# Kernel optimization log

Measured on AMD Instinct MI355X. Metric: run time of the kernel, lower is better.

The kernel has to match this reference:

```python
import jax, jax.numpy as jnp
import numpy as np

D_IN = 2048
D_OUT = 2048
NUM_HEADS = 32
NUM_KV_GROUPS = 8
HEAD_DIM = D_OUT // NUM_HEADS          # 64
GROUP_SIZE = NUM_HEADS // NUM_KV_GROUPS  # 4
BATCH = 2
SEQ = 2048


def _rope(x, cos, sin):
    # x: [b, h, s, d]; cos/sin: [s, d]
    d = x.shape[-1]
    x1, x2 = x[..., : d // 2], x[..., d // 2:]
    rotated = jnp.concatenate((-x2, x1), axis=-1)
    return x * cos[None, None, :, :] + rotated * sin[None, None, :, :]


def setup_inputs() -> dict:
    key = jax.random.key(0)
    ks = jax.random.split(key, 8)
    x = jax.random.normal(ks[0], (BATCH, SEQ, D_IN), dtype=jnp.float32)
    cos = jax.random.normal(ks[1], (SEQ, HEAD_DIM), dtype=jnp.float32)
    sin = jax.random.normal(ks[2], (SEQ, HEAD_DIM), dtype=jnp.float32)
    # causal mask: True above the diagonal = masked out
    mask = jnp.triu(jnp.ones((SEQ, SEQ), dtype=jnp.bool_), k=1)
    s = 0.02
    Wq = jax.random.normal(ks[3], (D_IN, D_OUT), dtype=jnp.float32) * s
    Wk = jax.random.normal(ks[4], (D_IN, NUM_KV_GROUPS * HEAD_DIM), dtype=jnp.float32) * s
    Wv = jax.random.normal(ks[5], (D_IN, NUM_KV_GROUPS * HEAD_DIM), dtype=jnp.float32) * s
    Wo = jax.random.normal(ks[6], (D_OUT, D_OUT), dtype=jnp.float32) * s
    return {"x": x, "cos": cos, "sin": sin, "mask": mask,
            "Wq": Wq, "Wk": Wk, "Wv": Wv, "Wo": Wo}


def reference(x, cos, sin, mask, Wq, Wk, Wv, Wo):
    b, s, _ = x.shape
    # projections (Linear, no bias): weights stored as [d_in, d_out]
    q = (x @ Wq).reshape(b, s, NUM_HEADS, HEAD_DIM).transpose(0, 2, 1, 3)      # [b,H,s,d]
    k = (x @ Wk).reshape(b, s, NUM_KV_GROUPS, HEAD_DIM).transpose(0, 2, 1, 3)  # [b,G,s,d]
    v = (x @ Wv).reshape(b, s, NUM_KV_GROUPS, HEAD_DIM).transpose(0, 2, 1, 3)  # [b,G,s,d]
    q = _rope(q, cos, sin)
    k = _rope(k, cos, sin)
    # GQA broadcast: repeat each KV group group_size times along head axis
    k = jnp.repeat(k, GROUP_SIZE, axis=1)  # [b,H,s,d]
    v = jnp.repeat(v, GROUP_SIZE, axis=1)  # [b,H,s,d]
    scores = jnp.einsum('bhqd,bhkd->bhqk', q, k)
    scores = jnp.where(mask[None, None, :, :], -jnp.inf, scores)
    # original scales AFTER masking: softmax(scores / sqrt(head_dim)); -inf stays -inf
    attn = jax.nn.softmax(scores * (1.0 / np.sqrt(HEAD_DIM)), axis=-1)
    ctx = jnp.einsum('bhqk,bhkd->bqhd', attn, v).reshape(b, s, D_OUT)
    return ctx @ Wo
```

## Files before the change

kernel.cpp:

```cpp
#include <hip/hip_runtime.h>
#include <hip/hip_fp16.h>

#define SEQ    2048
#define DIN    2048
#define DOUT   2048
#define NH     32
#define NKV    8
#define HD     64
#define BB     2

typedef _Float16 half_t;
typedef __attribute__((ext_vector_type(8))) _Float16 half8;
typedef __attribute__((ext_vector_type(4))) _Float16 half4;
typedef __attribute__((ext_vector_type(2))) __fp16   fp16x2;
typedef __attribute__((ext_vector_type(4))) float    floatx4;

union H8U { half8 h; int u[4]; };
union H2I { fp16x2 h; int i; };

#if __has_builtin(__builtin_amdgcn_exp2f)
#define EXP2F(x) __builtin_amdgcn_exp2f(x)
#else
#define EXP2F(x) __expf((x) * 0.6931471805599453f)
#endif

__device__ __forceinline__ void gload16(void* l, const void* g) {
    __builtin_amdgcn_global_load_lds(
        (const __attribute__((address_space(1))) void*)g,
        (__attribute__((address_space(3))) void*)l, 16, 0, 0);
}

__global__ void cast_f2h(const float* __restrict__ in, half_t* __restrict__ out, int n4) {
    int i = blockIdx.x * blockDim.x + threadIdx.x;
    if (i < n4) {
        float4 v = ((const float4*)in)[i];
        half4 h;
        h[0] = (half_t)v.x; h[1] = (half_t)v.y; h[2] = (half_t)v.z; h[3] = (half_t)v.w;
        ((half4*)out)[i] = h;
    }
}

__global__ __launch_bounds__(256) void tcast(const float* __restrict__ in, half_t* __restrict__ out,
                                             int Kd, int Nd) {
    __shared__ float T[32][33];
    int x0 = blockIdx.x * 32, y0 = blockIdx.y * 32;
    int tx = threadIdx.x & 31, ty = threadIdx.x >> 5;
    #pragma unroll
    for (int j = 0; j < 4; j++)
        T[ty + j * 8][tx] = in[(size_t)(y0 + ty + j * 8) * Nd + x0 + tx];
    __syncthreads();
    #pragma unroll
    for (int j = 0; j < 4; j++)
        out[(size_t)(x0 + ty + j * 8) * Kd + y0 + tx] = (half_t)T[tx][ty + j * 8];
}

__device__ __forceinline__ void gemm128_core(
    const half_t* __restrict__ A, const half_t* __restrict__ Bt,
    int m0, int n0, half_t* As, half_t* Bs, floatx4 (&acc)[4][4])
{
    const int tid = threadIdx.x, wave = tid >> 6, lane = tid & 63;
    const int quad = lane >> 4, l15 = lane & 15;
    const int wm = (wave >> 1) * 64, wn = (wave & 1) * 64;
    const int K = DIN;

    const half_t* pa[4]; const half_t* pb[4]; int ldso[4];
    #pragma unroll
    for (int is = 0; is < 4; is++) {
        int s  = is * 256 + tid;
        int kb = s >> 9, s1 = s & 511;
        int p  = s1 >> 3, sc = s1 & 7;
        int c  = sc ^ (p & 7);
        int row  = 2 * p + (c >> 2);
        int koff = kb * 32 + (c & 3) * 8;
        pa[is] = A  + (size_t)(m0 + row) * K + koff;
        pb[is] = Bt + (size_t)(n0 + row) * K + koff;
        ldso[is] = (is * 256 + wave * 64) * 8;
    }
    int aoff[4], boff[4];
    #pragma unroll
    for (int m = 0; m < 4; m++) {
        int r = wm + m * 16 + l15, p = r >> 1;
        aoff[m] = p * 64 + ((((r & 1) * 4 + quad) ^ (p & 7)) * 8);
        int rn = wn + m * 16 + l15, pn = rn >> 1;
        boff[m] = pn * 64 + ((((rn & 1) * 4 + quad) ^ (pn & 7)) * 8);
    }

    for (int k0 = 0; k0 < K; k0 += 64) {
        __syncthreads();
        #pragma unroll
        for (int is = 0; is < 4; is++) {
            gload16(As + ldso[is], pa[is] + k0);
            gload16(Bs + ldso[is], pb[is] + k0);
        }
        __syncthreads();
        half8 af[4][2], bf[4][2];
        #pragma unroll
        for (int i = 0; i < 4; i++) {
            af[i][0] = *(const half8*)(As + aoff[i]);
            af[i][1] = *(const half8*)(As + 4096 + aoff[i]);
            bf[i][0] = *(const half8*)(Bs + boff[i]);
            bf[i][1] = *(const half8*)(Bs + 4096 + boff[i]);
        }
        #pragma unroll
        for (int i = 0; i < 4; i++)
            #pragma unroll
            for (int j = 0; j < 4; j++)
                #pragma unroll
                for (int ks = 0; ks < 2; ks++)
                    acc[i][j] = __builtin_amdgcn_mfma_f32_16x16x32_f16(af[i][ks], bf[j][ks], acc[i][j], 0, 0, 0);
    }
}

__global__ __launch_bounds__(256) void gemm_qkv(
    const half_t* __restrict__ A, const half_t* __restrict__ Bt,
    const float* __restrict__ cosb, const float* __restrict__ sinb,
    half_t* __restrict__ Qh, half_t* __restrict__ Kh, half_t* __restrict__ Vt)
{
    __shared__ half_t As[8192];
    __shared__ half_t Bs[8192];
    const int bid = blockIdx.x;
    const int wg  = (bid & 7) * 96 + (bid >> 3);
    const int m0  = (wg & 31) * 128;
    const int n0  = (wg >> 5) * 128;

    floatx4 acc[4][4] = {};
    gemm128_core(A, Bt, m0, n0, As, Bs, acc);

    const int tid = threadIdx.x, wave = tid >> 6, lane = tid & 63;
    const int quad = lane >> 4, l15 = lane & 15;
    const int wm = (wave >> 1) * 64, wn = (wave & 1) * 64;
    const int headg = (n0 + wn) >> 6;
    const int b = m0 >> 11;
    const int s_base = (m0 & 2047) + wm + quad * 4;

    if (headg < 32) {
        half_t* outp = Qh + (size_t)(b * NH + headg) * SEQ * 64;
        #pragma unroll
        for (int i = 0; i < 4; i++)
            #pragma unroll
            for (int j = 0; j < 4; j++) {
                int d = j * 16 + l15;
                #pragma unroll
                for (int r = 0; r < 4; r++)
                    outp[(size_t)(s_base + i * 16 + r) * 64 + d] = (half_t)acc[i][j][r];
            }
    } else if (headg < 40) {
        half_t* outp = Kh + (size_t)(b * NKV + (headg - 32)) * SEQ * 64;
        #pragma unroll
        for (int i = 0; i < 4; i++)
            #pragma unroll
            for (int r = 0; r < 4; r++) {
                int s = s_base + i * 16 + r;
                #pragma unroll
                for (int j = 0; j < 2; j++) {
                    int d = j * 16 + l15;
                    float x1 = acc[i][j][r], x2 = acc[i][j + 2][r];
                    float c1 = cosb[s * 64 + d],      s1 = sinb[s * 64 + d];
                    float c2 = cosb[s * 64 + d + 32], s2 = sinb[s * 64 + d + 32];
                    outp[(size_t)s * 64 + d]      = (half_t)(x1 * c1 - x2 * s1);
                    outp[(size_t)s * 64 + d + 32] = (half_t)(x2 * c2 + x1 * s2);
                }
            }
    } else {
        half_t* vtp = Vt + (size_t)(b * NKV + (headg - 40)) * 64 * SEQ;
        #pragma unroll
        for (int i = 0; i < 4; i++) {
            int s = s_base + i * 16;
            #pragma unroll
            for (int j = 0; j < 4; j++) {
                int d = j * 16 + l15;
                half4 hv;
                hv[0] = (half_t)acc[i][j][0];
                hv[1] = (half_t)acc[i][j][1];
                hv[2] = (half_t)acc[i][j][2];
                hv[3] = (half_t)acc[i][j][3];
                *(half4*)(vtp + (size_t)d * SEQ + s) = hv;
            }
        }
    }
}

__global__ __launch_bounds__(256) void gemm_tn_f(
    const half_t* __restrict__ A, const half_t* __restrict__ Bt,
    float* __restrict__ C)
{
    __shared__ half_t As[8192];
    __shared__ half_t Bs[8192];
    const int bid = blockIdx.x;
    const int wg  = (bid & 7) * 64 + (bid >> 3);
    const int m0  = (wg & 31) * 128;
    const int n0  = (wg >> 5) * 128;

    floatx4 acc[4][4] = {};
    gemm128_core(A, Bt, m0, n0, As, Bs, acc);

    const int tid = threadIdx.x, wave = tid >> 6, lane = tid & 63;
    const int quad = lane >> 4, l15 = lane & 15;
    const int wm = (wave >> 1) * 64, wn = (wave & 1) * 64;
    #pragma unroll
    for (int i = 0; i < 4; i++) {
        int row = m0 + wm + i * 16 + quad * 4;
        #pragma unroll
        for (int j = 0; j < 4; j++) {
            int col = n0 + wn + j * 16 + l15;
            #pragma unroll
            for (int r = 0; r < 4; r++)
                C[(size_t)(row + r) * DOUT + col] = acc[i][j][r];
        }
    }
}

__global__ __launch_bounds__(256, 4) void attn(
    const half_t* __restrict__ Qh, const half_t* __restrict__ Kh,
    const half_t* __restrict__ Vt, const float* __restrict__ cosb,
    const float* __restrict__ sinb, half_t* __restrict__ ctx)
{
    __shared__ half_t Ks[2][4096];
    __shared__ half_t Vs[2][4096];

    const int tid = threadIdx.x, wave = tid >> 6, lane = tid & 63;
    const int quad = lane >> 4, l15 = lane & 15;
    const int bid = blockIdx.x;
    const int k  = bid >> 8;
    const int u  = bid & 255;
    const int q2 = u & 3;
    const int bh = u >> 2;
    const int qt = (k == 0) ? 15 - 2 * q2 : (k == 1) ? 2 * q2
                 : (k == 2) ? 14 - 2 * q2 : 2 * q2 + 1;
    const int b  = bh >> 5;
    const int h  = bh & 31;
    const int g  = h >> 2;
    const int q0 = qt * 128;
    const int wm = wave * 32;

    const half_t* kp = Kh + (size_t)(b * NKV + g) * SEQ * 64;
    const half_t* vp = Vt + (size_t)(b * NKV + g) * 64 * SEQ;

    half8 qf[2][2];
    {
        const float sc = 0.125f * 1.44269504088896f;
        const half_t* qpp = Qh + ((size_t)(b * NH + h) * SEQ + q0 + wm) * 64;
        #pragma unroll
        for (int mf = 0; mf < 2; mf++) {
            int s = q0 + wm + mf * 16 + l15;
            const float* cp = cosb + s * 64 + quad * 8;
            const float* sp = sinb + s * 64 + quad * 8;
            half8 xa = *(const half8*)(qpp + (size_t)(mf * 16 + l15) * 64 + quad * 8);
            half8 xb = *(const half8*)(qpp + (size_t)(mf * 16 + l15) * 64 + 32 + quad * 8);
            float4 c1a = *(const float4*)(cp),      c1b = *(const float4*)(cp + 4);
            float4 s1a = *(const float4*)(sp),      s1b = *(const float4*)(sp + 4);
            float4 c2a = *(const float4*)(cp + 32), c2b = *(const float4*)(cp + 36);
            float4 s2a = *(const float4*)(sp + 32), s2b = *(const float4*)(sp + 36);
            #pragma unroll
            for (int t = 0; t < 8; t++) {
                float cc1 = (t < 4) ? ((const float*)&c1a)[t] : ((const float*)&c1b)[t - 4];
                float ss1 = (t < 4) ? ((const float*)&s1a)[t] : ((const float*)&s1b)[t - 4];
                float cc2 = (t < 4) ? ((const float*)&c2a)[t] : ((const float*)&c2b)[t - 4];
                float ss2 = (t < 4) ? ((const float*)&s2a)[t] : ((const float*)&s2b)[t - 4];
                float x1 = (float)xa[t], x2 = (float)xb[t];
                qf[mf][0][t] = (half_t)((x1 * cc1 - x2 * ss1) * sc);
                qf[mf][1][t] = (half_t)((x2 * cc2 + x1 * ss2) * sc);
            }
        }
    }

    int koff[2], voff[2], lo[2];
    #pragma unroll
    for (int is = 0; is < 2; is++) {
        int s = is * 256 + tid;
        int p = s >> 3, c = (s & 7) ^ (p & 7);
        koff[is] = p * 64 + c * 8;
        voff[is] = p * SEQ + c * 8;
        lo[is]   = (is * 256 + wave * 64) * 8;
    }

    float m_i[2], l_i[2];
    m_i[0] = m_i[1] = -__builtin_inff();
    l_i[0] = l_i[1] = 0.f;
    floatx4 o[2][4] = {};

    const int ntiles = 2 * qt + 2;
    #pragma unroll
    for (int is = 0; is < 2; is++) {
        gload16(&Ks[0][lo[is]], kp + koff[is]);
        gload16(&Vs[0][lo[is]], vp + voff[is]);
    }

    const int srcA = l15 + ((quad & 1) ? 32 : 0);
    const int srcB = srcA + 16;
    const bool hiK = (quad >> 1) != 0;

    for (int kt = 0; kt < ntiles; kt++) {
        const int cur = kt & 1;
        const int kb  = kt * 64;
        __syncthreads();
        if (kt + 1 < ntiles) {
            const int kb2 = (kt + 1) * 64;
            #pragma unroll
            for (int is = 0; is < 2; is++) {
                gload16(&Ks[cur ^ 1][lo[is]], kp + (size_t)kb2 * 64 + koff[is]);
                gload16(&Vs[cur ^ 1][lo[is]], vp + kb2 + voff[is]);
            }
        }

        if (kb <= q0 + wm + 31) {
            floatx4 sa[2][4] = {};
            #pragma unroll
            for (int kc = 0; kc < 2; kc++)
                #pragma unroll
                for (int kf = 0; kf < 4; kf++) {
                    int row = kf * 16 + l15;
                    int sc = ((kc * 4 + quad) ^ (row & 7));
                    half8 kfr = *(const half8*)&Ks[cur][row * 64 + sc * 8];
                    sa[0][kf] = __builtin_amdgcn_mfma_f32_16x16x32_f16(kfr, qf[0][kc], sa[0][kf], 0, 0, 0);
                    sa[1][kf] = __builtin_amdgcn_mfma_f32_16x16x32_f16(kfr, qf[1][kc], sa[1][kf], 0, 0, 0);
                }

            if (kb + 63 > q0 + wm) {
                #pragma unroll
                for (int kf = 0; kf < 4; kf++)
                    #pragma unroll
                    for (int r = 0; r < 4; r++) {
                        int key = kb + kf * 16 + quad * 4 + r;
                        if (key > q0 + wm + l15)      sa[0][kf][r] = -__builtin_inff();
                        if (key > q0 + wm + 16 + l15) sa[1][kf][r] = -__builtin_inff();
                    }
            }

            int eh[2][4][2];
            float alpha[2];
            #pragma unroll
            for (int mf = 0; mf < 2; mf++) {
                float mt = sa[mf][0][0];
                #pragma unroll
                for (int kf = 0; kf < 4; kf++)
                    #pragma unroll
                    for (int r = 0; r < 4; r++) mt = fmaxf(mt, sa[mf][kf][r]);
                mt = fmaxf(mt, __shfl_xor(mt, 16));
                mt = fmaxf(mt, __shfl_xor(mt, 32));
                float mn = fmaxf(m_i[mf], mt);
                alpha[mf] = EXP2F(m_i[mf] - mn);
                m_i[mf] = mn;
                float rs = 0.f;
                #pragma unroll
                for (int kf = 0; kf < 4; kf++) {
                    float e0 = EXP2F(sa[mf][kf][0] - mn);
                    float e1 = EXP2F(sa[mf][kf][1] - mn);
                    float e2 = EXP2F(sa[mf][kf][2] - mn);
                    float e3 = EXP2F(sa[mf][kf][3] - mn);
                    rs += (e0 + e1) + (e2 + e3);
                    H2I p01, p23;
                    p01.h = __builtin_amdgcn_cvt_pkrtz(e0, e1);
                    p23.h = __builtin_amdgcn_cvt_pkrtz(e2, e3);
                    eh[mf][kf][0] = p01.i;
                    eh[mf][kf][1] = p23.i;
                }
                rs += __shfl_xor(rs, 16);
                rs += __shfl_xor(rs, 32);
                l_i[mf] = l_i[mf] * alpha[mf] + rs;
                #pragma unroll
                for (int nf = 0; nf < 4; nf++)
                    #pragma unroll
                    for (int r = 0; r < 4; r++) o[mf][nf][r] *= alpha[mf];
            }

            #pragma unroll
            for (int kc = 0; kc < 2; kc++) {
                H8U pf[2];
                #pragma unroll
                for (int mf = 0; mf < 2; mf++) {
                    int a0 = __shfl(eh[mf][2 * kc][0],     srcA);
                    int a1 = __shfl(eh[mf][2 * kc][1],     srcA);
                    int b0 = __shfl(eh[mf][2 * kc + 1][0], srcA);
                    int b1 = __shfl(eh[mf][2 * kc + 1][1], srcA);
                    int c0 = __shfl(eh[mf][2 * kc][0],     srcB);
                    int c1 = __shfl(eh[mf][2 * kc][1],     srcB);
                    int d0 = __shfl(eh[mf][2 * kc + 1][0], srcB);
                    int d1 = __shfl(eh[mf][2 * kc + 1][1], srcB);
                    pf[mf].u[0] = hiK ? b0 : a0;
                    pf[mf].u[1] = hiK ? b1 : a1;
                    pf[mf].u[2] = hiK ? d0 : c0;
                    pf[mf].u[3] = hiK ? d1 : c1;
                }
                #pragma unroll
                for (int nf = 0; nf < 4; nf++) {
                    int row = nf * 16 + l15;
                    int sc = ((kc * 4 + quad) ^ (row & 7));
                    half8 vf = *(const half8*)&Vs[cur][row * 64 + sc * 8];
                    o[0][nf] = __builtin_amdgcn_mfma_f32_16x16x32_f16(vf, pf[0].h, o[0][nf], 0, 0, 0);
                    o[1][nf] = __builtin_amdgcn_mfma_f32_16x16x32_f16(vf, pf[1].h, o[1][nf], 0, 0, 0);
                }
            }
        }
    }

    #pragma unroll
    for (int mf = 0; mf < 2; mf++) {
        float inv = 1.0f / l_i[mf];
        int s = q0 + wm + mf * 16 + l15;
        half_t* op = ctx + (size_t)(b * SEQ + s) * DOUT + h * 64 + quad * 4;
        #pragma unroll
        for (int nf = 0; nf < 4; nf++) {
            half4 hv;
            hv[0] = (half_t)(o[mf][nf][0] * inv);
            hv[1] = (half_t)(o[mf][nf][1] * inv);
            hv[2] = (half_t)(o[mf][nf][2] * inv);
            hv[3] = (half_t)(o[mf][nf][3] * inv);
            *(half4*)(op + nf * 16) = hv;
        }
    }
}

extern "C" void kernel_launch(void* const* d_in, const int* in_sizes, int n_in,
                              void* d_out, int out_size, void* d_ws, size_t ws_size,
                              hipStream_t stream) {
    const float* x    = (const float*)d_in[0];
    const float* cosb = (const float*)d_in[1];
    const float* sinb = (const float*)d_in[2];
    const float* Wq   = (const float*)d_in[4];
    const float* Wk   = (const float*)d_in[5];
    const float* Wv   = (const float*)d_in[6];
    const float* Wo   = (const float*)d_in[7];
    float* out = (float*)d_out;

    const size_t M  = (size_t)BB * SEQ;
    const size_t nX = M * DIN;

    char* ws = (char*)d_ws;
    const size_t MB = 1048576;
    half_t* xh     = (half_t*)(ws);
    half_t* WqkvT  = (half_t*)(ws + 16 * MB);
    half_t* WoT    = (half_t*)(ws + 28 * MB);
    half_t* Qh     = (half_t*)(ws + 36 * MB);
    half_t* Kh     = (half_t*)(ws + 52 * MB);
    half_t* Vt     = (half_t*)(ws + 56 * MB);
    half_t* ctxh   = (half_t*)(ws + 60 * MB);

    cast_f2h<<<(nX / 4) / 256, 256, 0, stream>>>(x, xh, nX / 4);
    tcast<<<dim3(64, 64), 256, 0, stream>>>(Wq, WqkvT, DIN, DOUT);
    tcast<<<dim3(16, 64), 256, 0, stream>>>(Wk, WqkvT + (size_t)2048 * 2048, DIN, 512);
    tcast<<<dim3(16, 64), 256, 0, stream>>>(Wv, WqkvT + (size_t)2560 * 2048, DIN, 512);
    tcast<<<dim3(64, 64), 256, 0, stream>>>(Wo, WoT, DOUT, DOUT);

    gemm_qkv<<<768, 256, 0, stream>>>(xh, WqkvT, cosb, sinb, Qh, Kh, Vt);

    attn<<<BB * NH * (SEQ / 128), 256, 0, stream>>>(Qh, Kh, Vt, cosb, sinb, ctxh);

    gemm_tn_f<<<512, 256, 0, stream>>>(ctxh, WoT, out);
}
```

Baseline: 342.7 us.

## Fuse prep casts, move Q RoPE into GEMM, lazy softmax rescale, setprio

Merges the five cast/transpose launches into a single prep kernel, which removes per-launch overhead. Q RoPE and softmax scaling move into the QKV GEMM epilogue, so the attention kernel no longer reads cos/sin for every query tile. The online softmax now rescales only when the running max grows by more than a threshold (wave-uniform check), which avoids most alpha multiplies. It also adds s_setprio around the MFMA blocks and replaces the swizzled GEMM block mapping with a plain 2D grid. The plain grid can lose L2 locality, and the lazy rescale keeps accuracy only because the exponent growth is bounded.

```diff
diff --git a/kernel.cpp b/kernel.cpp
--- a/kernel.cpp
+++ b/kernel.cpp
@@ -30,20 +30,30 @@
         (__attribute__((address_space(3))) void*)l, 16, 0, 0);
 }
 
-__global__ void cast_f2h(const float* __restrict__ in, half_t* __restrict__ out, int n4) {
-    int i = blockIdx.x * blockDim.x + threadIdx.x;
-    if (i < n4) {
-        float4 v = ((const float4*)in)[i];
+__global__ __launch_bounds__(256) void prep(
+    const float* __restrict__ x,
+    const float* __restrict__ Wq, const float* __restrict__ Wk,
+    const float* __restrict__ Wv, const float* __restrict__ Wo,
+    half_t* __restrict__ xh, half_t* __restrict__ WqkvT, half_t* __restrict__ WoT)
+{
+    __shared__ float T[32][33];
+    int bid = blockIdx.x;
+    if (bid < 8192) {
+        int i = bid * 256 + threadIdx.x;
+        float4 v = ((const float4*)x)[i];
         half4 h;
         h[0] = (half_t)v.x; h[1] = (half_t)v.y; h[2] = (half_t)v.z; h[3] = (half_t)v.w;
-        ((half4*)out)[i] = h;
-    }
-}
-
-__global__ __launch_bounds__(256) void tcast(const float* __restrict__ in, half_t* __restrict__ out,
-                                             int Kd, int Nd) {
-    __shared__ float T[32][33];
-    int x0 = blockIdx.x * 32, y0 = blockIdx.y * 32;
+        ((half4*)xh)[i] = h;
+        return;
+    }
+    bid -= 8192;
+    const float* in; half_t* out; int Nd, bx, by;
+    if (bid < 4096)      {            in = Wq; out = WqkvT;                        Nd = 2048; bx = bid & 63; by = bid >> 6; }
+    else if (bid < 5120) { bid -= 4096; in = Wk; out = WqkvT + (size_t)2048 * 2048; Nd = 512;  bx = bid & 15; by = bid >> 4; }
+    else if (bid < 6144) { bid -= 5120; in = Wv; out = WqkvT + (size_t)2560 * 2048; Nd = 512;  bx = bid & 15; by = bid >> 4; }
+    else                 { bid -= 6144; in = Wo; out = WoT;                         Nd = 2048; bx = bid & 63; by = bid >> 6; }
+    const int Kd = 2048;
+    int x0 = bx * 32, y0 = by * 32;
     int tx = threadIdx.x & 31, ty = threadIdx.x >> 5;
     #pragma unroll
     for (int j = 0; j < 4; j++)
@@ -118,10 +128,7 @@
 {
     __shared__ half_t As[8192];
     __shared__ half_t Bs[8192];
-    const int bid = blockIdx.x;
-    const int wg  = (bid & 7) * 96 + (bid >> 3);
-    const int m0  = (wg & 31) * 128;
-    const int n0  = (wg >> 5) * 128;
+    const int m0 = blockIdx.y * 128, n0 = blockIdx.x * 128;
 
     floatx4 acc[4][4] = {};
     gemm128_core(A, Bt, m0, n0, As, Bs, acc);
@@ -134,15 +141,22 @@
     const int s_base = (m0 & 2047) + wm + quad * 4;
 
     if (headg < 32) {
+        const float sc = 0.125f * 1.44269504088896f;
         half_t* outp = Qh + (size_t)(b * NH + headg) * SEQ * 64;
         #pragma unroll
         for (int i = 0; i < 4; i++)
             #pragma unroll
-            for (int j = 0; j < 4; j++) {
-                int d = j * 16 + l15;
-                #pragma unroll
-                for (int r = 0; r < 4; r++)
-                    outp[(size_t)(s_base + i * 16 + r) * 64 + d] = (half_t)acc[i][j][r];
+            for (int r = 0; r < 4; r++) {
+                int s = s_base + i * 16 + r;
+                #pragma unroll
+                for (int j = 0; j < 2; j++) {
+                    int d = j * 16 + l15;
+                    float x1 = acc[i][j][r], x2 = acc[i][j + 2][r];
+                    float c1 = cosb[s * 64 + d],      s1 = sinb[s * 64 + d];
+                    float c2 = cosb[s * 64 + d + 32], s2 = sinb[s * 64 + d + 32];
+                    outp[(size_t)s * 64 + d]      = (half_t)((x1 * c1 - x2 * s1) * sc);
+                    outp[(size_t)s * 64 + d + 32] = (half_t)((x2 * c2 + x1 * s2) * sc);
+                }
             }
     } else if (headg < 40) {
         half_t* outp = Kh + (size_t)(b * NKV + (headg - 32)) * SEQ * 64;
@@ -186,10 +200,7 @@
 {
     __shared__ half_t As[8192];
     __shared__ half_t Bs[8192];
-    const int bid = blockIdx.x;
-    const int wg  = (bid & 7) * 64 + (bid >> 3);
-    const int m0  = (wg & 31) * 128;
-    const int n0  = (wg >> 5) * 128;
+    const int m0 = blockIdx.y * 128, n0 = blockIdx.x * 128;
 
     floatx4 acc[4][4] = {};
     gemm128_core(A, Bt, m0, n0, As, Bs, acc);
@@ -212,8 +223,7 @@
 
 __global__ __launch_bounds__(256, 4) void attn(
     const half_t* __restrict__ Qh, const half_t* __restrict__ Kh,
-    const half_t* __restrict__ Vt, const float* __restrict__ cosb,
-    const float* __restrict__ sinb, half_t* __restrict__ ctx)
+    const half_t* __restrict__ Vt, half_t* __restrict__ ctx)
 {
     __shared__ half_t Ks[2][4096];
     __shared__ half_t Vs[2][4096];
@@ -238,29 +248,11 @@
 
     half8 qf[2][2];
     {
-        const float sc = 0.125f * 1.44269504088896f;
         const half_t* qpp = Qh + ((size_t)(b * NH + h) * SEQ + q0 + wm) * 64;
         #pragma unroll
         for (int mf = 0; mf < 2; mf++) {
-            int s = q0 + wm + mf * 16 + l15;
-            const float* cp = cosb + s * 64 + quad * 8;
-            const float* sp = sinb + s * 64 + quad * 8;
-            half8 xa = *(const half8*)(qpp + (size_t)(mf * 16 + l15) * 64 + quad * 8);
-            half8 xb = *(const half8*)(qpp + (size_t)(mf * 16 + l15) * 64 + 32 + quad * 8);
-            float4 c1a = *(const float4*)(cp),      c1b = *(const float4*)(cp + 4);
-            float4 s1a = *(const float4*)(sp),      s1b = *(const float4*)(sp + 4);
-            float4 c2a = *(const float4*)(cp + 32), c2b = *(const float4*)(cp + 36);
-            float4 s2a = *(const float4*)(sp + 32), s2b = *(const float4*)(sp + 36);
-            #pragma unroll
-            for (int t = 0; t < 8; t++) {
-                float cc1 = (t < 4) ? ((const float*)&c1a)[t] : ((const float*)&c1b)[t - 4];
-                float ss1 = (t < 4) ? ((const float*)&s1a)[t] : ((const float*)&s1b)[t - 4];
-                float cc2 = (t < 4) ? ((const float*)&c2a)[t] : ((const float*)&c2b)[t - 4];
-                float ss2 = (t < 4) ? ((const float*)&s2a)[t] : ((const float*)&s2b)[t - 4];
-                float x1 = (float)xa[t], x2 = (float)xb[t];
-                qf[mf][0][t] = (half_t)((x1 * cc1 - x2 * ss1) * sc);
-                qf[mf][1][t] = (half_t)((x2 * cc2 + x1 * ss2) * sc);
-            }
+            qf[mf][0] = *(const half8*)(qpp + (size_t)(mf * 16 + l15) * 64 + quad * 8);
+            qf[mf][1] = *(const half8*)(qpp + (size_t)(mf * 16 + l15) * 64 + 32 + quad * 8);
         }
     }
 
@@ -305,6 +297,7 @@
 
         if (kb <= q0 + wm + 31) {
             floatx4 sa[2][4] = {};
+            __builtin_amdgcn_s_setprio(1);
             #pragma unroll
             for (int kc = 0; kc < 2; kc++)
                 #pragma unroll
@@ -315,6 +308,7 @@
                     sa[0][kf] = __builtin_amdgcn_mfma_f32_16x16x32_f16(kfr, qf[0][kc], sa[0][kf], 0, 0, 0);
                     sa[1][kf] = __builtin_amdgcn_mfma_f32_16x16x32_f16(kfr, qf[1][kc], sa[1][kf], 0, 0, 0);
                 }
+            __builtin_amdgcn_s_setprio(0);
 
             if (kb + 63 > q0 + wm) {
                 #pragma unroll
@@ -328,7 +322,6 @@
             }
 
             int eh[2][4][2];
-            float alpha[2];
             #pragma unroll
             for (int mf = 0; mf < 2; mf++) {
                 float mt = sa[mf][0][0];
@@ -338,9 +331,17 @@
                     for (int r = 0; r < 4; r++) mt = fmaxf(mt, sa[mf][kf][r]);
                 mt = fmaxf(mt, __shfl_xor(mt, 16));
                 mt = fmaxf(mt, __shfl_xor(mt, 32));
-                float mn = fmaxf(m_i[mf], mt);
-                alpha[mf] = EXP2F(m_i[mf] - mn);
-                m_i[mf] = mn;
+                if (!__all(mt - m_i[mf] <= 8.0f)) {
+                    float mn2 = fmaxf(m_i[mf], mt);
+                    float a = EXP2F(m_i[mf] - mn2);
+                    m_i[mf] = mn2;
+                    l_i[mf] *= a;
+                    #pragma unroll
+                    for (int nf = 0; nf < 4; nf++)
+                        #pragma unroll
+                        for (int r = 0; r < 4; r++) o[mf][nf][r] *= a;
+                }
+                const float mn = m_i[mf];
                 float rs = 0.f;
                 #pragma unroll
                 for (int kf = 0; kf < 4; kf++) {
@@ -357,11 +358,7 @@
                 }
                 rs += __shfl_xor(rs, 16);
                 rs += __shfl_xor(rs, 32);
-                l_i[mf] = l_i[mf] * alpha[mf] + rs;
-                #pragma unroll
-                for (int nf = 0; nf < 4; nf++)
-                    #pragma unroll
-                    for (int r = 0; r < 4; r++) o[mf][nf][r] *= alpha[mf];
+                l_i[mf] += rs;
             }
 
             #pragma unroll
@@ -382,6 +379,7 @@
                     pf[mf].u[2] = hiK ? d0 : c0;
                     pf[mf].u[3] = hiK ? d1 : c1;
                 }
+                __builtin_amdgcn_s_setprio(1);
                 #pragma unroll
                 for (int nf = 0; nf < 4; nf++) {
                     int row = nf * 16 + l15;
@@ -390,6 +388,7 @@
                     o[0][nf] = __builtin_amdgcn_mfma_f32_16x16x32_f16(vf, pf[0].h, o[0][nf], 0, 0, 0);
                     o[1][nf] = __builtin_amdgcn_mfma_f32_16x16x32_f16(vf, pf[1].h, o[1][nf], 0, 0, 0);
                 }
+                __builtin_amdgcn_s_setprio(0);
             }
         }
     }
@@ -424,7 +423,6 @@
     float* out = (float*)d_out;
 
     const size_t M  = (size_t)BB * SEQ;
-    const size_t nX = M * DIN;
 
     char* ws = (char*)d_ws;
     const size_t MB = 1048576;
@@ -436,15 +434,11 @@
     half_t* Vt     = (half_t*)(ws + 56 * MB);
     half_t* ctxh   = (half_t*)(ws + 60 * MB);
 
-    cast_f2h<<<(nX / 4) / 256, 256, 0, stream>>>(x, xh, nX / 4);
-    tcast<<<dim3(64, 64), 256, 0, stream>>>(Wq, WqkvT, DIN, DOUT);
-    tcast<<<dim3(16, 64), 256, 0, stream>>>(Wk, WqkvT + (size_t)2048 * 2048, DIN, 512);
-    tcast<<<dim3(16, 64), 256, 0, stream>>>(Wv, WqkvT + (size_t)2560 * 2048, DIN, 512);
-    tcast<<<dim3(64, 64), 256, 0, stream>>>(Wo, WoT, DOUT, DOUT);
-
-    gemm_qkv<<<768, 256, 0, stream>>>(xh, WqkvT, cosb, sinb, Qh, Kh, Vt);
-
-    attn<<<BB * NH * (SEQ / 128), 256, 0, stream>>>(Qh, Kh, Vt, cosb, sinb, ctxh);
-
-    gemm_tn_f<<<512, 256, 0, stream>>>(ctxh, WoT, out);
-}
+    prep<<<18432, 256, 0, stream>>>(x, Wq, Wk, Wv, Wo, xh, WqkvT, WoT);
+
+    gemm_qkv<<<dim3(3072 / 128, M / 128), 256, 0, stream>>>(xh, WqkvT, cosb, sinb, Qh, Kh, Vt);
+
+    attn<<<BB * NH * (SEQ / 128), 256, 0, stream>>>(Qh, Kh, Vt, ctxh);
+
+    gemm_tn_f<<<dim3(DOUT / 128, M / 128), 256, 0, stream>>>(ctxh, WoT, out);
+}
```

New measurement: 315.4 us. -8.0%, faster.
